# Kernel tuning notes

Measured on AMD Instinct MI355X. Metric: run time of the kernel, lower is better.

The kernel has to match this reference:

```python
import jax, jax.numpy as jnp
import numpy as np

SHIFT = 1  # fixed choice for the random +/-1 shift_direction in the torch module


def setup_inputs() -> dict:
    key = jax.random.key(0)
    kx, kw = jax.random.split(key)
    x = jax.random.normal(kx, (128, 128, 56, 56), dtype=jnp.float32)
    W = jax.random.normal(kw, (32, 3, 2, 3, 4), dtype=jnp.float32)
    return {"x": x, "W": W}


def reference(x, W):
    n = x.shape[0]
    # sum-pool over a factor-2 split of the channel dim: (n,128,56,56)->(n,64,56,56)
    t = x.reshape(n, 2, 64, 56, 56).sum(axis=1)
    # view channels as (32 groups, 2): (n,32,2,56,56)
    t = t.reshape(n, 32, 2, 56, 56)
    # first torch unfold == size-3 zero-padded window along the 32-group axis
    tp = jnp.pad(t, ((0, 0), (1, 1), (0, 0), (0, 0), (0, 0)))
    w1 = jnp.stack([tp[:, i:i + 32] for i in range(3)], axis=1)  # (n,3,32,2,56,56)
    # circular shift along the last spatial axis (torch.roll on dim 5)
    w1 = jnp.roll(w1, SHIFT, axis=5)
    # second torch unfold == size-3 zero-padded window along the rolled 56 axis
    wp = jnp.pad(w1, ((0, 0), (0, 0), (0, 0), (0, 0), (0, 0), (1, 1)))
    w2 = jnp.stack([wp[..., l:l + 56] for l in range(3)], axis=5)  # (n,3,32,2,56,3,56)
    # grouped local-conv contraction; axes: n,i=win1(3),j=32,m=2,p=56,l=win2(3),o=56; k=4
    out = jnp.einsum('nijmplo,jimlk->njpok', w2, W)  # (n,32,56,56,4)
    t5 = out.transpose(0, 2, 3, 1, 4).reshape(n, 56, 56, 128)
    t5 = jnp.roll(t5, SHIFT, axis=1)  # roll along first spatial axis
    return t5.transpose(0, 3, 1, 2)  # (n,128,56,56)
```

## Files before the change

kernel.cpp:

```cpp
#include <hip/hip_runtime.h>

#define TPB 512

__global__ __launch_bounds__(TPB) void fused_shift_conv(const float* __restrict__ x,
                                                        const float* __restrict__ Wg,
                                                        float* __restrict__ out) {
    const int bid = blockIdx.x;
    const int ptile = bid % 28;
    const int n = bid / 28;
    const int p0 = ptile * 2;
    const int P0 = (p0 + 55) % 56;
    const int P1 = p0;

    __shared__ float4 sm4[128 * 15];

    const int tid = threadIdx.x;
    const int pl = tid >> 8;
    const int t8 = tid & 255;
    const int h = t8 & 1;
    const int c = t8 >> 1;
    const int j = c >> 2;
    const int k = c & 3;

    float wt[3][2][3];
#pragma unroll
    for (int i = 0; i < 3; ++i)
#pragma unroll
        for (int m = 0; m < 2; ++m)
#pragma unroll
            for (int l = 0; l < 3; ++l)
                wt[i][m][l] = Wg[(((j * 3 + i) * 2 + m) * 3 + l) * 4 + k];

    {
        const float4* x4 = reinterpret_cast<const float4*>(x);
#pragma unroll
        for (int it = 0; it < 4; ++it) {
            const int idx = tid + it * TPB;
            if (idx < 1792) {
                const int S = idx / 14;
                const int v = idx - S * 14;
                const int r = S >> 1;
                const int q = S & 1;
                const int Pq = q ? P1 : P0;
                const size_t base = (size_t)(n * 128 + r) * 784 + (size_t)Pq * 14 + (size_t)v;
                const float4 a = x4[base];
                const float4 b = x4[base + (size_t)64 * 784];
                float4 s;
                s.x = a.x + b.x; s.y = a.y + b.y; s.z = a.z + b.z; s.w = a.w + b.w;
                sm4[S * 15 + v] = s;
            }
        }
    }
    __syncthreads();

    const int q0 = h ? 6 : 13;
    const int qb = h ? 6 : -1;

    float acc[28];
#pragma unroll
    for (int u = 0; u < 28; ++u) acc[u] = 0.f;

#pragma unroll
    for (int i = 0; i < 3; ++i) {
        const int g = j + i - 1;
        if ((unsigned)g < 32u) {
#pragma unroll
            for (int m = 0; m < 2; ++m) {
                const float4* row4 = &sm4[((2 * g + m) * 2 + pl) * 15];
                float fe[32];
                {
                    const float4 t = row4[q0];
                    fe[0] = t.x; fe[1] = t.y; fe[2] = t.z; fe[3] = t.w;
                }
#pragma unroll
                for (int q = 1; q < 8; ++q) {
                    const float4 t = row4[qb + q];
                    fe[4 * q + 0] = t.x; fe[4 * q + 1] = t.y;
                    fe[4 * q + 2] = t.z; fe[4 * q + 3] = t.w;
                }
                float va[30];
#pragma unroll
                for (int d = 0; d < 30; ++d) va[d] = fe[d + 2];
                va[0]  = h ? va[0] : 0.f;
                va[29] = h ? 0.f : va[29];

                const float w0 = wt[i][m][0];
                const float w1 = wt[i][m][1];
                const float w2 = wt[i][m][2];
#pragma unroll
                for (int u = 0; u < 28; ++u)
                    acc[u] += w0 * va[u] + w1 * va[u + 1] + w2 * va[u + 2];
            }
        }
    }

    const int chalf = c >> 6;
    const int cr = c & 63;
    float4* o4 = reinterpret_cast<float4*>(out);

#pragma unroll
    for (int half = 0; half < 2; ++half) {
        __syncthreads();
        if (chalf == half) {
#pragma unroll
            for (int u4 = 0; u4 < 7; ++u4) {
                float4 v4;
                v4.x = acc[4 * u4 + 0];
                v4.y = acc[4 * u4 + 1];
                v4.z = acc[4 * u4 + 2];
                v4.w = acc[4 * u4 + 3];
                sm4[(cr + 64 * pl) * 15 + h * 7 + u4] = v4;
            }
        }
        __syncthreads();
#pragma unroll
        for (int it = 0; it < 4; ++it) {
            const int idx = tid + it * TPB;
            if (idx < 1792) {
                const int chp = idx / 14;
                const int v = idx - chp * 14;
                const int scr = chp & 63;
                const int spl = chp >> 6;
                o4[(size_t)(n * 128 + half * 64 + scr) * 784 + (size_t)(p0 + spl) * 14 + (size_t)v] =
                    sm4[chp * 15 + v];
            }
        }
    }
}

extern "C" void kernel_launch(void* const* d_in, const int* in_sizes, int n_in,
                              void* d_out, int out_size, void* d_ws, size_t ws_size,
                              hipStream_t stream) {
    const float* x = (const float*)d_in[0];
    const float* W = (const float*)d_in[1];
    float* out = (float*)d_out;
    const int n = in_sizes[0] / (128 * 56 * 56);
    const int grid = n * 28;
    fused_shift_conv<<<grid, TPB, 0, stream>>>(x, W, out);
}
```

Before: 97.40 us.

## Process two batch images per block with register prefetch of the second image

```diff
diff --git a/kernel.cpp b/kernel.cpp
--- a/kernel.cpp
+++ b/kernel.cpp
@@ -2,64 +2,12 @@
 
 #define TPB 512
 
-__global__ __launch_bounds__(TPB) void fused_shift_conv(const float* __restrict__ x,
-                                                        const float* __restrict__ Wg,
-                                                        float* __restrict__ out) {
-    const int bid = blockIdx.x;
-    const int ptile = bid % 28;
-    const int n = bid / 28;
-    const int p0 = ptile * 2;
-    const int P0 = (p0 + 55) % 56;
-    const int P1 = p0;
-
-    __shared__ float4 sm4[128 * 15];
-
-    const int tid = threadIdx.x;
-    const int pl = tid >> 8;
-    const int t8 = tid & 255;
-    const int h = t8 & 1;
-    const int c = t8 >> 1;
-    const int j = c >> 2;
-    const int k = c & 3;
-
-    float wt[3][2][3];
-#pragma unroll
-    for (int i = 0; i < 3; ++i)
-#pragma unroll
-        for (int m = 0; m < 2; ++m)
-#pragma unroll
-            for (int l = 0; l < 3; ++l)
-                wt[i][m][l] = Wg[(((j * 3 + i) * 2 + m) * 3 + l) * 4 + k];
-
-    {
-        const float4* x4 = reinterpret_cast<const float4*>(x);
-#pragma unroll
-        for (int it = 0; it < 4; ++it) {
-            const int idx = tid + it * TPB;
-            if (idx < 1792) {
-                const int S = idx / 14;
-                const int v = idx - S * 14;
-                const int r = S >> 1;
-                const int q = S & 1;
-                const int Pq = q ? P1 : P0;
-                const size_t base = (size_t)(n * 128 + r) * 784 + (size_t)Pq * 14 + (size_t)v;
-                const float4 a = x4[base];
-                const float4 b = x4[base + (size_t)64 * 784];
-                float4 s;
-                s.x = a.x + b.x; s.y = a.y + b.y; s.z = a.z + b.z; s.w = a.w + b.w;
-                sm4[S * 15 + v] = s;
-            }
-        }
-    }
-    __syncthreads();
-
-    const int q0 = h ? 6 : 13;
-    const int qb = h ? 6 : -1;
-
-    float acc[28];
+__device__ __forceinline__ void compute28(const float4* __restrict__ sm4,
+                                          const float wt[3][2][3],
+                                          int j, int pl, int q0, int qb, int h,
+                                          float acc[28]) {
 #pragma unroll
     for (int u = 0; u < 28; ++u) acc[u] = 0.f;
-
 #pragma unroll
     for (int i = 0; i < 3; ++i) {
         const int g = j + i - 1;
@@ -68,10 +16,7 @@
             for (int m = 0; m < 2; ++m) {
                 const float4* row4 = &sm4[((2 * g + m) * 2 + pl) * 15];
                 float fe[32];
-                {
-                    const float4 t = row4[q0];
-                    fe[0] = t.x; fe[1] = t.y; fe[2] = t.z; fe[3] = t.w;
-                }
+                { const float4 t = row4[q0]; fe[0] = t.x; fe[1] = t.y; fe[2] = t.z; fe[3] = t.w; }
 #pragma unroll
                 for (int q = 1; q < 8; ++q) {
                     const float4 t = row4[qb + q];
@@ -83,7 +28,6 @@
                 for (int d = 0; d < 30; ++d) va[d] = fe[d + 2];
                 va[0]  = h ? va[0] : 0.f;
                 va[29] = h ? 0.f : va[29];
-
                 const float w0 = wt[i][m][0];
                 const float w1 = wt[i][m][1];
                 const float w2 = wt[i][m][2];
@@ -93,11 +37,13 @@
             }
         }
     }
+}
 
+__device__ __forceinline__ void store2(float4* __restrict__ sm4, float4* __restrict__ o4,
+                                       const float acc[28], int tid, int c, int h, int pl,
+                                       int n, int p0) {
     const int chalf = c >> 6;
     const int cr = c & 63;
-    float4* o4 = reinterpret_cast<float4*>(out);
-
 #pragma unroll
     for (int half = 0; half < 2; ++half) {
         __syncthreads();
@@ -128,6 +74,107 @@
     }
 }
 
+__global__ __launch_bounds__(TPB) void fused_shift_conv(const float* __restrict__ x,
+                                                        const float* __restrict__ Wg,
+                                                        float* __restrict__ out) {
+    const int bid = blockIdx.x;
+    const int ptile = bid % 28;
+    const int n0 = (bid / 28) * 2;
+    const int p0 = ptile * 2;
+    const int P0 = (p0 + 55) % 56;
+    const int P1 = p0;
+
+    __shared__ float4 sm4[128 * 15];
+
+    const int tid = threadIdx.x;
+    const int pl = tid >> 8;
+    const int t8 = tid & 255;
+    const int h = t8 & 1;
+    const int c = t8 >> 1;
+    const int j = c >> 2;
+    const int k = c & 3;
+    const int q0 = h ? 6 : 13;
+    const int qb = h ? 6 : -1;
+
+    float wt[3][2][3];
+#pragma unroll
+    for (int i = 0; i < 3; ++i)
+#pragma unroll
+        for (int m = 0; m < 2; ++m)
+#pragma unroll
+            for (int l = 0; l < 3; ++l)
+                wt[i][m][l] = Wg[(((j * 3 + i) * 2 + m) * 3 + l) * 4 + k];
+
+    const float4* x4 = reinterpret_cast<const float4*>(x);
+
+#pragma unroll
+    for (int it = 0; it < 4; ++it) {
+        const int idx = tid + it * TPB;
+        if (idx < 1792) {
+            const int S = idx / 14;
+            const int v = idx - S * 14;
+            const int r = S >> 1;
+            const int q = S & 1;
+            const int Pq = q ? P1 : P0;
+            const size_t base = (size_t)(n0 * 128 + r) * 784 + (size_t)Pq * 14 + (size_t)v;
+            const float4 a = x4[base];
+            const float4 b = x4[base + (size_t)64 * 784];
+            float4 s;
+            s.x = a.x + b.x; s.y = a.y + b.y; s.z = a.z + b.z; s.w = a.w + b.w;
+            sm4[S * 15 + v] = s;
+        }
+    }
+
+    float4 pa[4], pb[4];
+#pragma unroll
+    for (int it = 0; it < 4; ++it) {
+        const int idx = tid + it * TPB;
+        if (idx < 1792) {
+            const int S = idx / 14;
+            const int v = idx - S * 14;
+            const int r = S >> 1;
+            const int q = S & 1;
+            const int Pq = q ? P1 : P0;
+            const size_t base = (size_t)((n0 + 1) * 128 + r) * 784 + (size_t)Pq * 14 + (size_t)v;
+            pa[it] = x4[base];
+            pb[it] = x4[base + (size_t)64 * 784];
+        }
+    }
+
+    __syncthreads();
+
+    float acc[28];
+    compute28(sm4, wt, j, pl, q0, qb, h, acc);
+
+#pragma unroll
+    for (int it = 0; it < 4; ++it) {
+        const int idx = tid + it * TPB;
+        if (idx < 1792) {
+            pa[it].x += pb[it].x; pa[it].y += pb[it].y;
+            pa[it].z += pb[it].z; pa[it].w += pb[it].w;
+        }
+    }
+
+    float4* o4 = reinterpret_cast<float4*>(out);
+    store2(sm4, o4, acc, tid, c, h, pl, n0, p0);
+
+    __syncthreads();
+
+#pragma unroll
+    for (int it = 0; it < 4; ++it) {
+        const int idx = tid + it * TPB;
+        if (idx < 1792) {
+            const int S = idx / 14;
+            const int v = idx - S * 14;
+            sm4[S * 15 + v] = pa[it];
+        }
+    }
+    __syncthreads();
+
+    compute28(sm4, wt, j, pl, q0, qb, h, acc);
+    store2(sm4, o4, acc, tid, c, h, pl, n0 + 1, p0);
+}
+
 extern "C" void kernel_launch(void* const* d_in, const int* in_sizes, int n_in,
                               void* d_out, int out_size, void* d_ws, size_t ws_size,
                               hipStream_t stream) {
@@ -135,6 +182,6 @@
     const float* W = (const float*)d_in[1];
     float* out = (float*)d_out;
     const int n = in_sizes[0] / (128 * 56 * 56);
-    const int grid = n * 28;
+    const int grid = (n / 2) * 28;
     fused_shift_conv<<<grid, TPB, 0, stream>>>(x, W, out);
 }
```

Measured after the change: 106.7 us. +9.6%, slower.
